# Performance work log

Hardware: AMD Instinct MI355X
Metric: run time of the kernel (lower is better)

## Reference

```python
import jax, jax.numpy as jnp
import numpy as np

EMB = 1024
HEADS = 16
DH = EMB // HEADS


def setup_inputs() -> dict:
    key = jax.random.key(0)
    ks = jax.random.split(key, 9)
    B, S = 4, 2048
    scale = 1.0 / np.sqrt(EMB)
    x = jax.random.normal(ks[0], (B, S, EMB), dtype=jnp.float32)
    Wq = jax.random.normal(ks[1], (EMB, EMB), dtype=jnp.float32) * scale
    Wk = jax.random.normal(ks[2], (EMB, EMB), dtype=jnp.float32) * scale
    Wv = jax.random.normal(ks[3], (EMB, EMB), dtype=jnp.float32) * scale
    Wo = jax.random.normal(ks[4], (EMB, EMB), dtype=jnp.float32) * scale
    bq = jnp.zeros((EMB,), jnp.float32)
    bk = jnp.zeros((EMB,), jnp.float32)
    bv = jnp.zeros((EMB,), jnp.float32)
    bo = jnp.zeros((EMB,), jnp.float32)
    return {"x": x, "Wq": Wq, "bq": bq, "Wk": Wk, "bk": bk,
            "Wv": Wv, "bv": bv, "Wo": Wo, "bo": bo}


def _split_heads(t):
    B, S, _ = t.shape
    return t.reshape(B, S, HEADS, DH).transpose(0, 2, 1, 3)  # [B,H,S,Dh]


def reference(x, Wq, bq, Wk, bk, Wv, bv, Wo, bo):
    q = _split_heads(x @ Wq + bq)
    k = _split_heads(x @ Wk + bk)
    v = _split_heads(x @ Wv + bv)
    # scaled dot-product attention, full [B,H,S,S] score matrix as in source
    logits = jnp.einsum("bhqd,bhkd->bhqk", q, k) / jnp.sqrt(jnp.float32(DH))
    attn = jax.nn.softmax(logits, axis=-1)
    ctx = jnp.einsum("bhqk,bhkd->bhqd", attn, v)
    B, _, S, _ = ctx.shape
    concat = ctx.transpose(0, 2, 1, 3).reshape(B, S, EMB)
    return concat @ Wo + bo
```

## Files before the change

### kernel.cpp

```cpp
#include <hip/hip_runtime.h>
#include <hip/hip_bf16.h>
#include <stdint.h>

typedef __bf16 bf16;
typedef __bf16 bf16x4 __attribute__((ext_vector_type(4)));
typedef __bf16 bf16x8 __attribute__((ext_vector_type(8)));
typedef float f32x4 __attribute__((ext_vector_type(4)));

__device__ __forceinline__ void async_ld16(const void* g, void* l) {
  __builtin_amdgcn_global_load_lds(
      (__attribute__((address_space(1))) void*)(void*)(g),
      (__attribute__((address_space(3))) void*)(l), 16, 0, 0);
}

__device__ __forceinline__ bf16 fast_bf16(float f) {
  uint32_t u = (__float_as_uint(f) + 0x8000u) >> 16;
  union { uint16_t s; bf16 b; } cv;
  cv.s = (uint16_t)u;
  return cv.b;
}

__device__ __forceinline__ uint32_t pack_bf16(float lo, float hi) {
  return __builtin_amdgcn_perm(__float_as_uint(hi) + 0x8000u,
                               __float_as_uint(lo) + 0x8000u, 0x07060302u);
}

__global__ __launch_bounds__(256) void cast_f32_bf16(const float* __restrict__ in,
                                                     bf16* __restrict__ out, int n) {
  int i = (blockIdx.x * 256 + threadIdx.x) * 4;
  if (i < n) {
    float4 f = *(const float4*)(in + i);
    uint2 o;
    o.x = pack_bf16(f.x, f.y);
    o.y = pack_bf16(f.z, f.w);
    *(uint2*)(out + i) = o;
  }
}

__global__ __launch_bounds__(256) void transpose_weights(const float* __restrict__ Wq,
                                                         const float* __restrict__ Wk,
                                                         const float* __restrict__ Wv,
                                                         const float* __restrict__ Wo,
                                                         bf16* __restrict__ Wt,
                                                         bf16* __restrict__ Wot) {
  __shared__ bf16 tile[64][66];
  int z = blockIdx.z;
  const float* src = z == 0 ? Wq : (z == 1 ? Wk : (z == 2 ? Wv : Wo));
  bf16* dst = z == 0 ? Wt : (z == 1 ? Wt + 1048576 : (z == 2 ? Wt + 2097152 : Wot));
  int r0 = blockIdx.x * 64, c0 = blockIdx.y * 64;
  int t = threadIdx.x;
#pragma unroll
  for (int i = 0; i < 16; ++i) {
    int idx = t + i * 256;
    int r = idx >> 6, c = idx & 63;
    tile[r][c] = fast_bf16(src[(size_t)(r0 + r) * 1024 + (c0 + c)]);
  }
  __syncthreads();
#pragma unroll
  for (int i = 0; i < 16; ++i) {
    int idx = t + i * 256;
    int c = idx >> 6, r = idx & 63;
    dst[(size_t)(c0 + c) * 1024 + (r0 + r)] = tile[r][c];
  }
}

__device__ __forceinline__ void gemm128_mainloop(const bf16* __restrict__ A,
                                                 const bf16* __restrict__ Bt, int K,
                                                 int rowBase, int colBase,
                                                 bf16* As, bf16* Bs,
                                                 f32x4 (&acc)[4][4]) {
  int t = threadIdx.x, lane = t & 63, w = t >> 6;
  int wM = w >> 1, wN = w & 1, quad = lane >> 4, l15 = lane & 15;
  int r_off = lane >> 3;
  int c_sw = (((lane & 7) ^ r_off) << 3);
  int sw = l15 & 7;
  for (int k0 = 0; k0 < K; k0 += 64) {
    __syncthreads();
#pragma unroll
    for (int i = 0; i < 4; ++i) {
      int e = i * 2048 + w * 512;
      int row = (e >> 6) + r_off;
      async_ld16(A + (size_t)(rowBase + row) * K + (k0 + c_sw), As + e);
      async_ld16(Bt + (size_t)(colBase + row) * K + (k0 + c_sw), Bs + e);
    }
    __syncthreads();
#pragma unroll
    for (int ks = 0; ks < 2; ++ks) {
      int co = (((ks * 4 + quad) ^ sw) << 3);
      bf16x8 af[4], bfr[4];
#pragma unroll
      for (int mi = 0; mi < 4; ++mi)
        af[mi] = *(const bf16x8*)(As + (wM * 64 + mi * 16 + l15) * 64 + co);
#pragma unroll
      for (int ni = 0; ni < 4; ++ni)
        bfr[ni] = *(const bf16x8*)(Bs + (wN * 64 + ni * 16 + l15) * 64 + co);
#pragma unroll
      for (int mi = 0; mi < 4; ++mi)
#pragma unroll
        for (int ni = 0; ni < 4; ++ni)
          acc[mi][ni] = __builtin_amdgcn_mfma_f32_16x16x32_bf16(af[mi], bfr[ni], acc[mi][ni], 0, 0, 0);
    }
  }
}

__global__ __launch_bounds__(256) void gemm_qkv(const bf16* __restrict__ X,
                                                const bf16* __restrict__ Wt,
                                                const float* __restrict__ bq,
                                                const float* __restrict__ bk,
                                                const float* __restrict__ bv,
                                                bf16* __restrict__ Qo,
                                                bf16* __restrict__ Ko,
                                                bf16* __restrict__ Vto) {
  __shared__ alignas(16) bf16 As[128 * 64];
  __shared__ alignas(16) bf16 Bs[128 * 64];
  f32x4 acc[4][4];
  f32x4 z = {0.f, 0.f, 0.f, 0.f};
#pragma unroll
  for (int mi = 0; mi < 4; ++mi)
#pragma unroll
    for (int ni = 0; ni < 4; ++ni) acc[mi][ni] = z;
  int rowBase = blockIdx.x * 128, colBase = blockIdx.y * 128;
  gemm128_mainloop(X, Wt, 1024, rowBase, colBase, As, Bs, acc);

  int t = threadIdx.x, lane = t & 63, w = t >> 6;
  int wM = w >> 1, wN = w & 1, quad = lane >> 4, l15 = lane & 15;
  int which = colBase >> 10;

  if (which == 2) {
#pragma unroll
    for (int mi = 0; mi < 4; ++mi)
#pragma unroll
      for (int ni = 0; ni < 4; ++ni) {
        int n = colBase + wN * 64 + ni * 16 + l15;
        int e = n & 1023;
        int h = e >> 6, d = e & 63;
        float bb = bv[e];
        int m0 = rowBase + wM * 64 + mi * 16 + quad * 4;
        int b = m0 >> 11, s = m0 & 2047;
        uint2 pv;
        pv.x = pack_bf16(acc[mi][ni][0] + bb, acc[mi][ni][1] + bb);
        pv.y = pack_bf16(acc[mi][ni][2] + bb, acc[mi][ni][3] + bb);
        *(uint2*)(Vto + (((size_t)((b << 4) + h) * 64 + d) << 11) + s) = pv;
      }
  } else {
    const float* bias = which == 0 ? bq : bk;
    bf16* dst = which == 0 ? Qo : Ko;
    float scale = which == 0 ? 0.125f * 1.44269504f : 1.0f;
#pragma unroll
    for (int mi = 0; mi < 4; ++mi)
#pragma unroll
      for (int ni = 0; ni < 4; ++ni) {
        int n = colBase + wN * 64 + ni * 16 + l15;
        int e = n & 1023;
        int h = e >> 6, d = e & 63;
        float bb = bias[e];
#pragma unroll
        for (int r = 0; r < 4; ++r) {
          int m = rowBase + wM * 64 + mi * 16 + quad * 4 + r;
          int b = m >> 11, s = m & 2047;
          dst[(((size_t)((b << 4) + h) * 2048 + s) << 6) + d] =
              fast_bf16((acc[mi][ni][r] + bb) * scale);
        }
      }
  }
}

__global__ __launch_bounds__(256) void gemm_out(const bf16* __restrict__ Cb,
                                                const bf16* __restrict__ Wot,
                                                const float* __restrict__ bo,
                                                float* __restrict__ out) {
  __shared__ alignas(16) bf16 As[128 * 64];
  __shared__ alignas(16) bf16 Bs[128 * 64];
  f32x4 acc[4][4];
  f32x4 z = {0.f, 0.f, 0.f, 0.f};
#pragma unroll
  for (int mi = 0; mi < 4; ++mi)
#pragma unroll
    for (int ni = 0; ni < 4; ++ni) acc[mi][ni] = z;
  int rowBase = blockIdx.x * 128, colBase = blockIdx.y * 128;
  gemm128_mainloop(Cb, Wot, 1024, rowBase, colBase, As, Bs, acc);

  int t = threadIdx.x, lane = t & 63, w = t >> 6;
  int wM = w >> 1, wN = w & 1, quad = lane >> 4, l15 = lane & 15;
#pragma unroll
  for (int mi = 0; mi < 4; ++mi)
#pragma unroll
    for (int ni = 0; ni < 4; ++ni) {
      int n = colBase + wN * 64 + ni * 16 + l15;
      float bb = bo[n];
#pragma unroll
      for (int r = 0; r < 4; ++r) {
        int m = rowBase + wM * 64 + mi * 16 + quad * 4 + r;
        out[(size_t)m * 1024 + n] = acc[mi][ni][r] + bb;
      }
    }
}

__global__ __launch_bounds__(256) void attn(const bf16* __restrict__ Q,
                                            const bf16* __restrict__ Kg,
                                            const bf16* __restrict__ Vt,
                                            bf16* __restrict__ ctx) {
  __shared__ alignas(16) bf16 QPs[128 * 64];
  __shared__ alignas(16) bf16 Ks[64 * 64];
  __shared__ alignas(16) bf16 Vs[64 * 64];

  int t = threadIdx.x, lane = t & 63, w = t >> 6;
  int quad = lane >> 4, l15 = lane & 15;
  int r_off = lane >> 3;
  int c_sw = (((lane & 7) ^ r_off) << 3);
  int sw = l15 & 7;
  int bh = blockIdx.y;
  int q0 = blockIdx.x * 128;
  const bf16* Qp = Q + ((size_t)bh * 2048 + q0) * 64;
  const bf16* Kp = Kg + (size_t)bh * 2048 * 64;
  const bf16* Vp = Vt + (size_t)bh * 64 * 2048;

#pragma unroll
  for (int i = 0; i < 4; ++i) {
    int e = i * 2048 + w * 512;
    int row = (e >> 6) + r_off;
    async_ld16(Qp + row * 64 + c_sw, QPs + e);
  }
  __syncthreads();

  bf16x8 qf[2][2];
#pragma unroll
  for (int ks = 0; ks < 2; ++ks)
#pragma unroll
    for (int qi = 0; qi < 2; ++qi)
      qf[ks][qi] = *(const bf16x8*)(QPs + (w * 32 + qi * 16 + l15) * 64 + (((ks * 4 + quad) ^ sw) << 3));

  bf16* Ps = QPs + w * 2048;

  f32x4 o[2][4];
  f32x4 z = {0.f, 0.f, 0.f, 0.f};
  float lpart[2] = {0.f, 0.f};
#pragma unroll
  for (int mi = 0; mi < 2; ++mi)
#pragma unroll
    for (int ni = 0; ni < 4; ++ni) o[mi][ni] = z;

  for (int kt = 0; kt < 2048; kt += 64) {
    __syncthreads();
#pragma unroll
    for (int i = 0; i < 2; ++i) {
      int e = w * 1024 + i * 512;
      int row = (e >> 6) + r_off;
      async_ld16(Kp + (size_t)(kt + row) * 64 + c_sw, Ks + e);
      async_ld16(Vp + (size_t)row * 2048 + kt + c_sw, Vs + e);
    }
    __syncthreads();

    f32x4 sc[4][2];
#pragma unroll
    for (int ki = 0; ki < 4; ++ki)
#pragma unroll
      for (int qi = 0; qi < 2; ++qi) sc[ki][qi] = z;
#pragma unroll
    for (int ks = 0; ks < 2; ++ks) {
      int co = (((ks * 4 + quad) ^ sw) << 3);
      bf16x8 kf[4];
#pragma unroll
      for (int ki = 0; ki < 4; ++ki)
        kf[ki] = *(const bf16x8*)(Ks + (ki * 16 + l15) * 64 + co);
#pragma unroll
      for (int ki = 0; ki < 4; ++ki)
#pragma unroll
        for (int qi = 0; qi < 2; ++qi)
          sc[ki][qi] = __builtin_amdgcn_mfma_f32_16x16x32_bf16(kf[ki], qf[ks][qi], sc[ki][qi], 0, 0, 0);
    }

#pragma unroll
    for (int qi = 0; qi < 2; ++qi)
#pragma unroll
      for (int ki = 0; ki < 4; ++ki) {
        float p0 = __builtin_amdgcn_exp2f(sc[ki][qi][0]);
        float p1 = __builtin_amdgcn_exp2f(sc[ki][qi][1]);
        float p2 = __builtin_amdgcn_exp2f(sc[ki][qi][2]);
        float p3 = __builtin_amdgcn_exp2f(sc[ki][qi][3]);
        lpart[qi] += (p0 + p1) + (p2 + p3);
        uint2 pb;
        pb.x = pack_bf16(p0, p1);
        pb.y = pack_bf16(p2, p3);
        int cs = (ki * 2 + (quad >> 1)) ^ sw;
        *(uint2*)(Ps + (qi * 16 + l15) * 64 + cs * 8 + (quad & 1) * 4) = pb;
      }

    asm volatile("s_waitcnt lgkmcnt(0)" ::: "memory");

#pragma unroll
    for (int ks = 0; ks < 2; ++ks) {
      int co = (((ks * 4 + quad) ^ sw) << 3);
      bf16x8 pf[2], vf[4];
#pragma unroll
      for (int mi = 0; mi < 2; ++mi)
        pf[mi] = *(const bf16x8*)(Ps + (mi * 16 + l15) * 64 + co);
#pragma unroll
      for (int ni = 0; ni < 4; ++ni)
        vf[ni] = *(const bf16x8*)(Vs + (ni * 16 + l15) * 64 + co);
#pragma unroll
      for (int mi = 0; mi < 2; ++mi)
#pragma unroll
        for (int ni = 0; ni < 4; ++ni)
          o[mi][ni] = __builtin_amdgcn_mfma_f32_16x16x32_bf16(pf[mi], vf[ni], o[mi][ni], 0, 0, 0);
    }
  }

  int b = bh >> 4, h = bh & 15;
#pragma unroll
  for (int mi = 0; mi < 2; ++mi) {
    float l = lpart[mi];
    l += __shfl_xor(l, 16, 64);
    l += __shfl_xor(l, 32, 64);
    float rl[4];
#pragma unroll
    for (int r = 0; r < 4; ++r) rl[r] = 1.0f / __shfl(l, quad * 4 + r, 64);
#pragma unroll
    for (int ni = 0; ni < 4; ++ni) {
      int col = h * 64 + ni * 16 + l15;
#pragma unroll
      for (int r = 0; r < 4; ++r) {
        int q = q0 + w * 32 + mi * 16 + quad * 4 + r;
        ctx[(size_t)(b * 2048 + q) * 1024 + col] = fast_bf16(o[mi][ni][r] * rl[r]);
      }
    }
  }
}

extern "C" void kernel_launch(void* const* d_in, const int* in_sizes, int n_in,
                              void* d_out, int out_size, void* d_ws, size_t ws_size,
                              hipStream_t stream) {
  const float* x  = (const float*)d_in[0];
  const float* Wq = (const float*)d_in[1];
  const float* bq = (const float*)d_in[2];
  const float* Wk = (const float*)d_in[3];
  const float* bk = (const float*)d_in[4];
  const float* Wv = (const float*)d_in[5];
  const float* bv = (const float*)d_in[6];
  const float* Wo = (const float*)d_in[7];
  const float* bo = (const float*)d_in[8];
  float* out = (float*)d_out;

  char* ws = (char*)d_ws;
  const size_t MB = 1048576;
  bf16* xb  = (bf16*)(ws);
  bf16* Wt  = (bf16*)(ws + 16 * MB);
  bf16* Wot = (bf16*)(ws + 22 * MB);
  bf16* Qb  = (bf16*)(ws + 24 * MB);
  bf16* Kb  = (bf16*)(ws + 40 * MB);
  bf16* Vtb = (bf16*)(ws + 56 * MB);
  bf16* Cx  = (bf16*)(ws + 72 * MB);

  cast_f32_bf16<<<8192, 256, 0, stream>>>(x, xb, 8388608);
  transpose_weights<<<dim3(16, 16, 4), 256, 0, stream>>>(Wq, Wk, Wv, Wo, Wt, Wot);
  gemm_qkv<<<dim3(64, 24, 1), 256, 0, stream>>>(xb, Wt, bq, bk, bv, Qb, Kb, Vtb);
  attn<<<dim3(16, 64, 1), 256, 0, stream>>>(Qb, Kb, Vtb, Cx);
  gemm_out<<<dim3(64, 8, 1), 256, 0, stream>>>(Cx, Wot, bo, out);
}
```

Measured before the change: 298.8 us.

## Double-buffer K/V tiles and halve attention query tile to 64 rows

The attention kernel now preloads the first K/V tile together with Q, then prefetches the next K/V tile into a second LDS buffer while computing the current one, leaving one barrier per iteration instead of two. The query tile per block shrinks from 128 to 64 rows (16 per wave), doubling the grid to 2048 blocks. This is meant to hide global-load latency and raise occupancy. In exchange each K/V tile is reused by half as many queries, so K/V global traffic doubles and there is less MFMA work per LDS fragment load.

```diff
diff --git a/kernel.cpp b/kernel.cpp
--- a/kernel.cpp
+++ b/kernel.cpp
@@ -200,9 +200,9 @@
                                             const bf16* __restrict__ Kg,
                                             const bf16* __restrict__ Vt,
                                             bf16* __restrict__ ctx) {
-  __shared__ alignas(16) bf16 QPs[128 * 64];
-  __shared__ alignas(16) bf16 Ks[64 * 64];
-  __shared__ alignas(16) bf16 Vs[64 * 64];
+  __shared__ alignas(16) bf16 QPs[64 * 64];
+  __shared__ alignas(16) bf16 Ks[2][64 * 64];
+  __shared__ alignas(16) bf16 Vs[2][64 * 64];
 
   int t = threadIdx.x, lane = t & 63, w = t >> 6;
   int quad = lane >> 4, l15 = lane & 15;
@@ -210,119 +210,109 @@
   int c_sw = (((lane & 7) ^ r_off) << 3);
   int sw = l15 & 7;
   int bh = blockIdx.y;
-  int q0 = blockIdx.x * 128;
+  int q0 = blockIdx.x * 64;
   const bf16* Qp = Q + ((size_t)bh * 2048 + q0) * 64;
   const bf16* Kp = Kg + (size_t)bh * 2048 * 64;
   const bf16* Vp = Vt + (size_t)bh * 64 * 2048;
 
 #pragma unroll
-  for (int i = 0; i < 4; ++i) {
-    int e = i * 2048 + w * 512;
+  for (int i = 0; i < 2; ++i) {
+    int e = w * 1024 + i * 512;
     int row = (e >> 6) + r_off;
     async_ld16(Qp + row * 64 + c_sw, QPs + e);
+    async_ld16(Kp + (size_t)row * 64 + c_sw, Ks[0] + e);
+    async_ld16(Vp + (size_t)row * 2048 + c_sw, Vs[0] + e);
   }
   __syncthreads();
 
-  bf16x8 qf[2][2];
+  bf16x8 qf[2];
 #pragma unroll
   for (int ks = 0; ks < 2; ++ks)
-#pragma unroll
-    for (int qi = 0; qi < 2; ++qi)
-      qf[ks][qi] = *(const bf16x8*)(QPs + (w * 32 + qi * 16 + l15) * 64 + (((ks * 4 + quad) ^ sw) << 3));
-
-  bf16* Ps = QPs + w * 2048;
-
-  f32x4 o[2][4];
+    qf[ks] = *(const bf16x8*)(QPs + (w * 16 + l15) * 64 + (((ks * 4 + quad) ^ sw) << 3));
+  asm volatile("s_waitcnt lgkmcnt(0)" ::: "memory");
+
+  bf16* Ps = QPs + w * 1024;
+
+  f32x4 o[4];
   f32x4 z = {0.f, 0.f, 0.f, 0.f};
-  float lpart[2] = {0.f, 0.f};
-#pragma unroll
-  for (int mi = 0; mi < 2; ++mi)
-#pragma unroll
-    for (int ni = 0; ni < 4; ++ni) o[mi][ni] = z;
-
-  for (int kt = 0; kt < 2048; kt += 64) {
-    __syncthreads();
-#pragma unroll
-    for (int i = 0; i < 2; ++i) {
-      int e = w * 1024 + i * 512;
-      int row = (e >> 6) + r_off;
-      async_ld16(Kp + (size_t)(kt + row) * 64 + c_sw, Ks + e);
-      async_ld16(Vp + (size_t)row * 2048 + kt + c_sw, Vs + e);
-    }
-    __syncthreads();
-
-    f32x4 sc[4][2];
-#pragma unroll
-    for (int ki = 0; ki < 4; ++ki)
-#pragma unroll
-      for (int qi = 0; qi < 2; ++qi) sc[ki][qi] = z;
+  float lpart = 0.f;
+#pragma unroll
+  for (int ni = 0; ni < 4; ++ni) o[ni] = z;
+
+  for (int kt = 0; kt < 32; ++kt) {
+    int cur = kt & 1;
+    if (kt < 31) {
+      int kn = (kt + 1) * 64;
+#pragma unroll
+      for (int i = 0; i < 2; ++i) {
+        int e = w * 1024 + i * 512;
+        int row = (e >> 6) + r_off;
+        async_ld16(Kp + (size_t)(kn + row) * 64 + c_sw, Ks[cur ^ 1] + e);
+        async_ld16(Vp + (size_t)row * 2048 + kn + c_sw, Vs[cur ^ 1] + e);
+      }
+    }
+
+    f32x4 sc[4];
+#pragma unroll
+    for (int ki = 0; ki < 4; ++ki) sc[ki] = z;
 #pragma unroll
     for (int ks = 0; ks < 2; ++ks) {
       int co = (((ks * 4 + quad) ^ sw) << 3);
       bf16x8 kf[4];
 #pragma unroll
       for (int ki = 0; ki < 4; ++ki)
-        kf[ki] = *(const bf16x8*)(Ks + (ki * 16 + l15) * 64 + co);
+        kf[ki] = *(const bf16x8*)(Ks[cur] + (ki * 16 + l15) * 64 + co);
 #pragma unroll
       for (int ki = 0; ki < 4; ++ki)
-#pragma unroll
-        for (int qi = 0; qi < 2; ++qi)
-          sc[ki][qi] = __builtin_amdgcn_mfma_f32_16x16x32_bf16(kf[ki], qf[ks][qi], sc[ki][qi], 0, 0, 0);
-    }
-
-#pragma unroll
-    for (int qi = 0; qi < 2; ++qi)
-#pragma unroll
-      for (int ki = 0; ki < 4; ++ki) {
-        float p0 = __builtin_amdgcn_exp2f(sc[ki][qi][0]);
-        float p1 = __builtin_amdgcn_exp2f(sc[ki][qi][1]);
-        float p2 = __builtin_amdgcn_exp2f(sc[ki][qi][2]);
-        float p3 = __builtin_amdgcn_exp2f(sc[ki][qi][3]);
-        lpart[qi] += (p0 + p1) + (p2 + p3);
-        uint2 pb;
-        pb.x = pack_bf16(p0, p1);
-        pb.y = pack_bf16(p2, p3);
-        int cs = (ki * 2 + (quad >> 1)) ^ sw;
-        *(uint2*)(Ps + (qi * 16 + l15) * 64 + cs * 8 + (quad & 1) * 4) = pb;
-      }
+        sc[ki] = __builtin_amdgcn_mfma_f32_16x16x32_bf16(kf[ki], qf[ks], sc[ki], 0, 0, 0);
+    }
+
+#pragma unroll
+    for (int ki = 0; ki < 4; ++ki) {
+      float p0 = __builtin_amdgcn_exp2f(sc[ki][0]);
+      float p1 = __builtin_amdgcn_exp2f(sc[ki][1]);
+      float p2 = __builtin_amdgcn_exp2f(sc[ki][2]);
+      float p3 = __builtin_amdgcn_exp2f(sc[ki][3]);
+      lpart += (p0 + p1) + (p2 + p3);
+      uint2 pb;
+      pb.x = pack_bf16(p0, p1);
+      pb.y = pack_bf16(p2, p3);
+      int cs = (ki * 2 + (quad >> 1)) ^ sw;
+      *(uint2*)(Ps + l15 * 64 + cs * 8 + (quad & 1) * 4) = pb;
+    }
 
     asm volatile("s_waitcnt lgkmcnt(0)" ::: "memory");
 
 #pragma unroll
     for (int ks = 0; ks < 2; ++ks) {
       int co = (((ks * 4 + quad) ^ sw) << 3);
-      bf16x8 pf[2], vf[4];
-#pragma unroll
-      for (int mi = 0; mi < 2; ++mi)
-        pf[mi] = *(const bf16x8*)(Ps + (mi * 16 + l15) * 64 + co);
+      bf16x8 pf = *(const bf16x8*)(Ps + l15 * 64 + co);
+      bf16x8 vf[4];
 #pragma unroll
       for (int ni = 0; ni < 4; ++ni)
-        vf[ni] = *(const bf16x8*)(Vs + (ni * 16 + l15) * 64 + co);
-#pragma unroll
-      for (int mi = 0; mi < 2; ++mi)
-#pragma unroll
-        for (int ni = 0; ni < 4; ++ni)
-          o[mi][ni] = __builtin_amdgcn_mfma_f32_16x16x32_bf16(pf[mi], vf[ni], o[mi][ni], 0, 0, 0);
-    }
+        vf[ni] = *(const bf16x8*)(Vs[cur] + (ni * 16 + l15) * 64 + co);
+#pragma unroll
+      for (int ni = 0; ni < 4; ++ni)
+        o[ni] = __builtin_amdgcn_mfma_f32_16x16x32_bf16(pf, vf[ni], o[ni], 0, 0, 0);
+    }
+
+    __syncthreads();
   }
 
   int b = bh >> 4, h = bh & 15;
-#pragma unroll
-  for (int mi = 0; mi < 2; ++mi) {
-    float l = lpart[mi];
-    l += __shfl_xor(l, 16, 64);
-    l += __shfl_xor(l, 32, 64);
-    float rl[4];
-#pragma unroll
-    for (int r = 0; r < 4; ++r) rl[r] = 1.0f / __shfl(l, quad * 4 + r, 64);
-#pragma unroll
-    for (int ni = 0; ni < 4; ++ni) {
-      int col = h * 64 + ni * 16 + l15;
-#pragma unroll
-      for (int r = 0; r < 4; ++r) {
-        int q = q0 + w * 32 + mi * 16 + quad * 4 + r;
-        ctx[(size_t)(b * 2048 + q) * 1024 + col] = fast_bf16(o[mi][ni][r] * rl[r]);
-      }
+  float l = lpart;
+  l += __shfl_xor(l, 16, 64);
+  l += __shfl_xor(l, 32, 64);
+  float rl[4];
+#pragma unroll
+  for (int r = 0; r < 4; ++r) rl[r] = 1.0f / __shfl(l, quad * 4 + r, 64);
+#pragma unroll
+  for (int ni = 0; ni < 4; ++ni) {
+    int col = h * 64 + ni * 16 + l15;
+#pragma unroll
+    for (int r = 0; r < 4; ++r) {
+      int q = q0 + w * 16 + quad * 4 + r;
+      ctx[(size_t)(b * 2048 + q) * 1024 + col] = fast_bf16(o[ni][r] * rl[r]);
     }
   }
 }
@@ -354,6 +344,6 @@
   cast_f32_bf16<<<8192, 256, 0, stream>>>(x, xb, 8388608);
   transpose_weights<<<dim3(16, 16, 4), 256, 0, stream>>>(Wq, Wk, Wv, Wo, Wt, Wot);
   gemm_qkv<<<dim3(64, 24, 1), 256, 0, stream>>>(xb, Wt, bq, bk, bv, Qb, Kb, Vtb);
-  attn<<<dim3(16, 64, 1), 256, 0, stream>>>(Qb, Kb, Vtb, Cx);
+  attn<<<dim3(32, 64, 1), 256, 0, stream>>>(Qb, Kb, Vtb, Cx);
   gemm_out<<<dim3(64, 8, 1), 256, 0, stream>>>(Cx, Wot, bo, out);
 }
```

Measured after the change: 306.0 us. 2.4% more time.
